# Kernel optimization log

Hardware: AMD Instinct MI355X
Metric: run time of the kernel (lower is better)

Reference implementation:

```python
import jax, jax.numpy as jnp
import numpy as np

B, S, H = 2, 2048, 2048
NH, NG = 16, 4           # attention heads, query groups
HD = H // NH             # head_dim = 128
HPG = NH // NG           # heads per group = 4


def setup_inputs() -> dict:
    key = jax.random.key(0)
    ks = jax.random.split(key, 8)
    s = 0.02
    return {
        "hidden_states": jax.random.normal(ks[0], (B, S, H), dtype=jnp.float32),
        "attention_mask": jnp.ones((B, S), dtype=jnp.int32),
        "Wq": jax.random.normal(ks[1], (H, H), dtype=jnp.float32) * s,
        "bq": jnp.zeros((H,), dtype=jnp.float32),
        "Wk": jax.random.normal(ks[2], (HD * NG, H), dtype=jnp.float32) * s,
        "bk": jnp.zeros((HD * NG,), dtype=jnp.float32),
        "Wv": jax.random.normal(ks[3], (HD * NG, H), dtype=jnp.float32) * s,
        "bv": jnp.zeros((HD * NG,), dtype=jnp.float32),
    }


def reference(hidden_states, attention_mask, Wq, bq, Wk, bk, Wv, bv):
    b, s, _ = hidden_states.shape
    scale = 1.0 / np.sqrt(HD).astype(np.float32)
    # projections (torch Linear: x @ W.T + b)
    q = hidden_states @ Wq.T + bq                      # [b,s,H]
    k = hidden_states @ Wk.T + bk                      # [b,s,NG*HD]
    v = hidden_states @ Wv.T + bv
    # q grouped so that repeat_interleave of k/v along heads == broadcast over heads_per_group
    q = q.reshape(b, s, NG, HPG, HD)                   # heads = group-major order
    k = k.reshape(b, s, NG, HD)
    v = v.reshape(b, s, NG, HD)
    scores = jnp.einsum("bsgpd,btgd->bgpst", q, k) * scale  # [b,NG,HPG,s,s]
    # mask: positions with attention_mask == 0 get finfo.min added
    mask_add = jnp.where(attention_mask == 0,
                         jnp.finfo(scores.dtype).min,
                         jnp.float32(0.0))             # [b,t]
    scores = scores + mask_add[:, None, None, None, :]
    attn = jax.nn.softmax(scores, axis=-1)             # dropout is identity in eval
    out = jnp.einsum("bgpst,btgd->bsgpd", attn, v)     # [b,s,NG,HPG,HD]
    return out.reshape(b, s, NH * HD)
```

## Files before the change

### kernel.cpp

```cpp
#include <hip/hip_runtime.h>
#include <hip/hip_bf16.h>

#define B_ 2
#define S_ 2048
#define H_ 2048
#define NH_ 16
#define NG_ 4
#define HD_ 128
#define HPG_ 4

typedef __attribute__((ext_vector_type(8))) short short8;
typedef __attribute__((ext_vector_type(4))) short short4v;
typedef __attribute__((ext_vector_type(4))) float float4v;

#define MFMA_BF16 __builtin_amdgcn_mfma_f32_16x16x32_bf16

#if __has_builtin(__builtin_amdgcn_exp2f)
#define EXP2(x) __builtin_amdgcn_exp2f(x)
#else
#define EXP2(x) exp2f(x)
#endif

__device__ __forceinline__ void gload16(const void* g, void* l) {
    __builtin_amdgcn_global_load_lds(
        (const __attribute__((address_space(1))) unsigned int*)g,
        (__attribute__((address_space(3))) unsigned int*)l, 16, 0, 0);
}

__device__ __forceinline__ short bf16bits(float f) {
    union { __hip_bfloat16 h; short s; } u;
    u.h = __float2bfloat16(f);
    return u.s;
}

__global__ __launch_bounds__(256) void cvt_all(const float* __restrict__ hs,
                                               const float* __restrict__ wq,
                                               const float* __restrict__ wk,
                                               const float* __restrict__ wv,
                                               const int* __restrict__ mask,
                                               const float* __restrict__ bq,
                                               const float* __restrict__ bk,
                                               const float* __restrict__ bv,
                                               __hip_bfloat16* __restrict__ o_hs,
                                               __hip_bfloat16* __restrict__ o_wq,
                                               __hip_bfloat16* __restrict__ o_wk,
                                               __hip_bfloat16* __restrict__ o_wv,
                                               float* __restrict__ o_m,
                                               float* __restrict__ o_bc) {
    int i = blockIdx.x * 256 + threadIdx.x;
    if (blockIdx.x == 0) {
#pragma unroll
        for (int j = 0; j < 16; ++j) {
            int idx = threadIdx.x * 16 + j;
            o_m[idx] = mask[idx] ? 0.0f : -3.0e38f;
        }
    }
    if (blockIdx.x == 1) {
#pragma unroll
        for (int j = 0; j < 12; ++j) {
            int idx = j * 256 + threadIdx.x;
            float v = (idx < 2048) ? bq[idx] : (idx < 2560) ? bk[idx - 2048] : bv[idx - 2560];
            o_bc[idx] = v;
        }
    }
    const float* src;
    __hip_bfloat16* dst;
    int off;
    if (i < 1048576)      { src = hs; dst = o_hs; off = i; }
    else if (i < 1572864) { src = wq; dst = o_wq; off = i - 1048576; }
    else if (i < 1703936) { src = wk; dst = o_wk; off = i - 1572864; }
    else                  { src = wv; dst = o_wv; off = i - 1703936; }
    const float4* s4 = (const float4*)src;
    float4 a = s4[2 * (size_t)off];
    float4 b = s4[2 * (size_t)off + 1];
    union { short8 s; __hip_bfloat16 h[8]; } u;
    u.h[0] = __float2bfloat16(a.x); u.h[1] = __float2bfloat16(a.y);
    u.h[2] = __float2bfloat16(a.z); u.h[3] = __float2bfloat16(a.w);
    u.h[4] = __float2bfloat16(b.x); u.h[5] = __float2bfloat16(b.y);
    u.h[6] = __float2bfloat16(b.z); u.h[7] = __float2bfloat16(b.w);
    *(short8*)(dst + 8 * (size_t)off) = u.s;
}

__global__ __launch_bounds__(512, 2) void gemm_qkv3(const __hip_bfloat16* __restrict__ A,
                                                    const __hip_bfloat16* __restrict__ Wcat,
                                                    const float* __restrict__ biasC,
                                                    __hip_bfloat16* __restrict__ qO,
                                                    __hip_bfloat16* __restrict__ kO,
                                                    __hip_bfloat16* __restrict__ vTO) {
    extern __shared__ char lds[];

    const int tid = threadIdx.x;
    const int lane = tid & 63;
    const int x = lane & 15, g = lane >> 4;
    const int wid = tid >> 6;
    const int wm = wid >> 2, wn = wid & 3;

    const int id0 = blockIdx.x;
    const int id = ((id0 & 7) << 5) | (id0 >> 3);
    const int bn_t = id >> 4, bm_t = id & 15;
    const int bm = bm_t * 256, bn = bn_t * 192;
    const int K = 2048;

    const int srow = tid >> 2;
    const int schunk = (tid & 3) ^ ((tid >> 3) & 3);
    const __hip_bfloat16* gA0 = A + (size_t)(bm + srow) * K + schunk * 8;
    const __hip_bfloat16* gA1 = A + (size_t)(bm + 128 + srow) * K + schunk * 8;
    const __hip_bfloat16* gB0 = Wcat + (size_t)(bn + srow) * K + schunk * 8;
    const __hip_bfloat16* gB1 = Wcat + (size_t)(bn + 128 + srow) * K + schunk * 8;
    const bool doB1 = (tid < 256);

    const int xk = (x >> 1) & 3;
    int aoffA[8], boffB[3];
#pragma unroll
    for (int mb = 0; mb < 8; ++mb)
        aoffA[mb] = (wm * 128 + mb * 16 + x) * 64 + ((g ^ xk) * 16);
#pragma unroll
    for (int nb = 0; nb < 3; ++nb)
        boffB[nb] = 16384 + (wn * 48 + nb * 16 + x) * 64 + ((g ^ xk) * 16);

    float4v acc[8][3];
#pragma unroll
    for (int i = 0; i < 8; ++i)
#pragma unroll
        for (int j = 0; j < 3; ++j) acc[i][j] = (float4v)0.f;

#pragma unroll
    for (int p = 0; p < 2; ++p) {
        char* stg = lds + p * 28672;
        gload16(gA0, stg + tid * 16);
        gload16(gA1, stg + 8192 + tid * 16);
        gload16(gB0, stg + 16384 + tid * 16);
        if (doB1) gload16(gB1, stg + 24576 + tid * 16);
        gA0 += 32; gA1 += 32; gB0 += 32; gB1 += 32;
    }
    if (doB1) asm volatile("s_waitcnt vmcnt(4)" ::: "memory");
    else      asm volatile("s_waitcnt vmcnt(3)" ::: "memory");
    __builtin_amdgcn_s_barrier();

#pragma unroll 4
    for (int t = 0; t < 64; ++t) {
        const char* bc = lds + (t & 3) * 28672;
        char* stg = lds + ((t + 2) & 3) * 28672;

        short8 afA[4], bfr[3];
#pragma unroll
        for (int mb = 0; mb < 4; ++mb) afA[mb] = *(const short8*)(bc + aoffA[mb]);
#pragma unroll
        for (int nb = 0; nb < 3; ++nb) bfr[nb] = *(const short8*)(bc + boffB[nb]);
        if (t < 62) {
            gload16(gA0, stg + tid * 16);
            gload16(gA1, stg + 8192 + tid * 16);
            gA0 += 32; gA1 += 32;
        }
        __builtin_amdgcn_s_barrier();
        asm volatile("s_waitcnt lgkmcnt(0)");
        __builtin_amdgcn_sched_barrier(0);
        __builtin_amdgcn_s_setprio(1);
#pragma unroll
        for (int mb = 0; mb < 4; ++mb)
#pragma unroll
            for (int nb = 0; nb < 3; ++nb)
                acc[mb][nb] = MFMA_BF16(afA[mb], bfr[nb], acc[mb][nb], 0, 0, 0);
        __builtin_amdgcn_s_setprio(0);
        __builtin_amdgcn_s_barrier();

        short8 afB[4];
#pragma unroll
        for (int mb = 0; mb < 4; ++mb) afB[mb] = *(const short8*)(bc + aoffA[4 + mb]);
        if (t < 62) {
            gload16(gB0, stg + 16384 + tid * 16);
            if (doB1) gload16(gB1, stg + 24576 + tid * 16);
            gB0 += 32; gB1 += 32;
        }
        __builtin_amdgcn_s_barrier();
        asm volatile("s_waitcnt lgkmcnt(0)");
        __builtin_amdgcn_sched_barrier(0);
        __builtin_amdgcn_s_setprio(1);
#pragma unroll
        for (int mb = 0; mb < 4; ++mb)
#pragma unroll
            for (int nb = 0; nb < 3; ++nb)
                acc[4 + mb][nb] = MFMA_BF16(afB[mb], bfr[nb], acc[4 + mb][nb], 0, 0, 0);
        __builtin_amdgcn_s_setprio(0);
        if (t < 62) {
            if (doB1) asm volatile("s_waitcnt vmcnt(4)" ::: "memory");
            else      asm volatile("s_waitcnt vmcnt(3)" ::: "memory");
        } else {
            asm volatile("s_waitcnt vmcnt(0)" ::: "memory");
        }
        __builtin_amdgcn_s_barrier();
    }

#pragma unroll
    for (int mb = 0; mb < 8; ++mb) {
#pragma unroll
        for (int nb = 0; nb < 3; ++nb) {
            const int n = bn + wn * 48 + nb * 16 + x;
            const float bsv = biasC[n];
            const int m0 = bm + wm * 128 + mb * 16 + g * 4;
            if (n < 2048) {
#pragma unroll
                for (int r = 0; r < 4; ++r)
                    qO[(size_t)(m0 + r) * 2048 + n] = __float2bfloat16(acc[mb][nb][r] + bsv);
            } else if (n < 2560) {
                const int nk = n - 2048;
#pragma unroll
                for (int r = 0; r < 4; ++r)
                    kO[(size_t)(m0 + r) * 512 + nk] = __float2bfloat16(acc[mb][nb][r] + bsv);
            } else {
                const int nv = n - 2560;
                const int gv = nv >> 7, d = nv & 127;
                const int bb2 = m0 >> 11, s = m0 & 2047;
                short4v pk;
#pragma unroll
                for (int r = 0; r < 4; ++r) pk[r] = bf16bits(acc[mb][nb][r] + bsv);
                *(short4v*)(vTO + ((size_t)(bb2 * NG_ + gv) * HD_ + d) * S_ + s) = pk;
            }
        }
    }
}

__global__ __launch_bounds__(512, 2) void attn(const __hip_bfloat16* __restrict__ q,
                                               const __hip_bfloat16* __restrict__ k,
                                               const __hip_bfloat16* __restrict__ vT,
                                               const float* __restrict__ M,
                                               float* __restrict__ out) {
    extern __shared__ char smem[];
    char* Ks = smem;
    char* Vs = smem + 16384;
    char* Ps = smem + 32768;

    const int tid = threadIdx.x;
    const int lane = tid & 63;
    const int w = tid >> 6;
    const int wm = w >> 2, wn = w & 3;
    const int x = lane & 15, g = lane >> 4;

    const int bid0 = blockIdx.x;
    const int bid = ((bid0 & 7) << 5) | (bid0 >> 3);
    const int qt = bid & 7;
    const int hp = (bid >> 3) & 3;
    const int gi = (bid >> 5) & 3;
    const int b = bid >> 7;
    const int head = gi * HPG_ + hp;
    const int q0 = qt * 256;

    short8 qf[4][4];
#pragma unroll
    for (int nb = 0; nb < 4; ++nb) {
        const int qq = q0 + wn * 64 + nb * 16 + x;
        const __hip_bfloat16* qrow = q + ((size_t)(b * S_ + qq) * NH_ + head) * HD_ + g * 8;
#pragma unroll
        for (int ks = 0; ks < 4; ++ks)
            qf[nb][ks] = *(const short8*)(qrow + ks * 32);
    }

    const int kchunk = (tid & 15) ^ ((tid >> 4) & 15);
    const __hip_bfloat16* kp = k + ((size_t)(b * S_ + (tid >> 4)) * NG_ + gi) * HD_ + kchunk * 8;
    const int vchunk = (tid & 7) ^ ((tid >> 3) & 7);
    const __hip_bfloat16* vp = vT + ((size_t)(b * NG_ + gi) * HD_ + (tid >> 3)) * S_ + vchunk * 8;
    const float* mp = M + b * S_ + wm * 32 + g * 4;

    float4v O[4][4];
#pragma unroll
    for (int i = 0; i < 4; ++i)
#pragma unroll
        for (int j = 0; j < 4; ++j) O[i][j] = (float4v)0.f;
    float l_part[4] = {0.f, 0.f, 0.f, 0.f};

    const float SM = 0.08838834764831845f * 1.4426950408889634f;

    gload16(kp, Ks + tid * 16);
    gload16(kp + 16384, Ks + tid * 16 + 8192);
    kp += 32768;

    for (int it = 0; it < 32; ++it) {
        __syncthreads();
        float4 mv0 = *(const float4*)(mp);
        float4 mv1 = *(const float4*)(mp + 16);
        mp += 64;
        gload16(vp, Vs + tid * 16);
        gload16(vp + 131072, Vs + tid * 16 + 8192);
        vp += 64;

        float4v sc[2][4];
#pragma unroll
        for (int i = 0; i < 2; ++i)
#pragma unroll
            for (int j = 0; j < 4; ++j) sc[i][j] = (float4v)0.f;
        __builtin_amdgcn_s_setprio(1);
#pragma unroll
        for (int ks = 0; ks < 4; ++ks) {
            short8 af0 = *(const short8*)(Ks + (wm * 32 + x) * 256 + (((ks * 4 + g) ^ x) * 16));
            short8 af1 = *(const short8*)(Ks + (wm * 32 + 16 + x) * 256 + (((ks * 4 + g) ^ x) * 16));
#pragma unroll
            for (int nb = 0; nb < 4; ++nb) {
                sc[0][nb] = MFMA_BF16(af0, qf[nb][ks], sc[0][nb], 0, 0, 0);
                sc[1][nb] = MFMA_BF16(af1, qf[nb][ks], sc[1][nb], 0, 0, 0);
            }
        }
        __builtin_amdgcn_s_setprio(0);

#pragma unroll
        for (int mb = 0; mb < 2; ++mb) {
            const float4 mv = mb ? mv1 : mv0;
            const int hs = wm * 8 + mb * 4 + g;
#pragma unroll
            for (int nb = 0; nb < 4; ++nb) {
                float p0 = EXP2(fmaf(sc[mb][nb][0], SM, mv.x));
                float p1 = EXP2(fmaf(sc[mb][nb][1], SM, mv.y));
                float p2 = EXP2(fmaf(sc[mb][nb][2], SM, mv.z));
                float p3 = EXP2(fmaf(sc[mb][nb][3], SM, mv.w));
                l_part[nb] += (p0 + p1) + (p2 + p3);
                short4v pk;
                pk[0] = bf16bits(p0); pk[1] = bf16bits(p1);
                pk[2] = bf16bits(p2); pk[3] = bf16bits(p3);
                *(short4v*)(Ps + (wn * 64 + nb * 16 + x) * 136 + hs * 8) = pk;
            }
        }

        __syncthreads();
        if (it < 31) {
            gload16(kp, Ks + tid * 16);
            gload16(kp + 16384, Ks + tid * 16 + 8192);
            kp += 32768;
        }

#pragma unroll
        for (int ks = 0; ks < 2; ++ks) {
            short8 vf[4], pf[4];
#pragma unroll
            for (int i4 = 0; i4 < 4; ++i4) {
                vf[i4] = *(const short8*)(Vs + (wm * 64 + i4 * 16 + x) * 128 +
                                          (((ks * 4 + g) ^ (x & 7)) * 16));
                const char* pb = Ps + (wn * 64 + i4 * 16 + x) * 136 + (8 * ks + 2 * g) * 8;
                union { short4v h[2]; short8 s8; } uu;
                uu.h[0] = *(const short4v*)pb;
                uu.h[1] = *(const short4v*)(pb + 8);
                pf[i4] = uu.s8;
            }
            __builtin_amdgcn_s_setprio(1);
#pragma unroll
            for (int mb = 0; mb < 4; ++mb)
#pragma unroll
                for (int nb = 0; nb < 4; ++nb)
                    O[mb][nb] = MFMA_BF16(vf[mb], pf[nb], O[mb][nb], 0, 0, 0);
            __builtin_amdgcn_s_setprio(0);
        }
    }

    __syncthreads();
#pragma unroll
    for (int nb = 0; nb < 4; ++nb) {
        l_part[nb] += __shfl_xor(l_part[nb], 16);
        l_part[nb] += __shfl_xor(l_part[nb], 32);
    }
    float* lws = (float*)Ps;
    if (g == 0) {
#pragma unroll
        for (int nb = 0; nb < 4; ++nb)
            lws[wm * 256 + wn * 64 + nb * 16 + x] = l_part[nb];
    }
    __syncthreads();
    float inv[4];
#pragma unroll
    for (int nb = 0; nb < 4; ++nb)
        inv[nb] = 1.0f / (l_part[nb] + lws[(wm ^ 1) * 256 + wn * 64 + nb * 16 + x]);

#pragma unroll
    for (int mb = 0; mb < 4; ++mb) {
#pragma unroll
        for (int nb = 0; nb < 4; ++nb) {
            const int qq = q0 + wn * 64 + nb * 16 + x;
            const int d0 = wm * 64 + mb * 16 + g * 4;
            float4v o = O[mb][nb] * inv[nb];
            *(float4v*)(out + (size_t)(b * S_ + qq) * H_ + head * HD_ + d0) = o;
        }
    }
}

extern "C" void kernel_launch(void* const* d_in, const int* in_sizes, int n_in,
                              void* d_out, int out_size, void* d_ws, size_t ws_size,
                              hipStream_t stream) {
    (void)in_sizes; (void)n_in; (void)out_size; (void)ws_size;
    const float* hs = (const float*)d_in[0];
    const int* amask = (const int*)d_in[1];
    const float* Wq = (const float*)d_in[2];
    const float* bq = (const float*)d_in[3];
    const float* Wk = (const float*)d_in[4];
    const float* bk = (const float*)d_in[5];
    const float* Wv = (const float*)d_in[6];
    const float* bv = (const float*)d_in[7];
    float* out = (float*)d_out;

    char* ws = (char*)d_ws;
    __hip_bfloat16* hsB = (__hip_bfloat16*)(ws);
    __hip_bfloat16* WqB = (__hip_bfloat16*)(ws + 16777216);
    __hip_bfloat16* WkB = (__hip_bfloat16*)(ws + 25165824);
    __hip_bfloat16* WvB = (__hip_bfloat16*)(ws + 27262976);
    __hip_bfloat16* qB  = (__hip_bfloat16*)(ws + 29360128);
    __hip_bfloat16* kB  = (__hip_bfloat16*)(ws + 46137344);
    __hip_bfloat16* vTB = (__hip_bfloat16*)(ws + 50331648);
    float* Mf           = (float*)(ws + 54525952);
    float* biasC        = (float*)(ws + 54542336);

    hipFuncSetAttribute((const void*)gemm_qkv3,
                        hipFuncAttributeMaxDynamicSharedMemorySize, 114688);
    hipFuncSetAttribute((const void*)attn,
                        hipFuncAttributeMaxDynamicSharedMemorySize, 67584);

    cvt_all<<<7168, 256, 0, stream>>>(hs, Wq, Wk, Wv, amask, bq, bk, bv,
                                      hsB, WqB, WkB, WvB, Mf, biasC);
    gemm_qkv3<<<256, 512, 114688, stream>>>(hsB, WqB, biasC, qB, kB, vTB);
    attn<<<256, 512, 67584, stream>>>(qB, kB, vTB, Mf, out);
}
```

Baseline: 232.7 us.

## Software-pipeline attention loop with double-buffered K, V and P tiles

Restructures the attention main loop so the QK^T and softmax for tile i run alongside the PV product for tile i-1. K, V and P get double buffers in LDS, which removes the second __syncthreads per iteration and lets loads for the next tile overlap compute. A prologue and epilogue handle the first and last tiles. LDS use roughly doubles to about 132 KB, so only one block fits per CU. With a 256-block grid this may not cost occupancy in practice.

```diff
diff --git a/kernel.cpp b/kernel.cpp
--- a/kernel.cpp
+++ b/kernel.cpp
@@ -227,8 +227,8 @@
                                                float* __restrict__ out) {
     extern __shared__ char smem[];
     char* Ks = smem;
-    char* Vs = smem + 16384;
-    char* Ps = smem + 32768;
+    char* Vs = smem + 32768;
+    char* Ps = smem + 65536;
 
     const int tid = threadIdx.x;
     const int lane = tid & 63;
@@ -267,23 +267,11 @@
 #pragma unroll
         for (int j = 0; j < 4; ++j) O[i][j] = (float4v)0.f;
     float l_part[4] = {0.f, 0.f, 0.f, 0.f};
+    float4v sc[2][4];
 
     const float SM = 0.08838834764831845f * 1.4426950408889634f;
 
-    gload16(kp, Ks + tid * 16);
-    gload16(kp + 16384, Ks + tid * 16 + 8192);
-    kp += 32768;
-
-    for (int it = 0; it < 32; ++it) {
-        __syncthreads();
-        float4 mv0 = *(const float4*)(mp);
-        float4 mv1 = *(const float4*)(mp + 16);
-        mp += 64;
-        gload16(vp, Vs + tid * 16);
-        gload16(vp + 131072, Vs + tid * 16 + 8192);
-        vp += 64;
-
-        float4v sc[2][4];
+    auto QKf = [&](const char* KsC) {
 #pragma unroll
         for (int i = 0; i < 2; ++i)
 #pragma unroll
@@ -291,8 +279,8 @@
         __builtin_amdgcn_s_setprio(1);
 #pragma unroll
         for (int ks = 0; ks < 4; ++ks) {
-            short8 af0 = *(const short8*)(Ks + (wm * 32 + x) * 256 + (((ks * 4 + g) ^ x) * 16));
-            short8 af1 = *(const short8*)(Ks + (wm * 32 + 16 + x) * 256 + (((ks * 4 + g) ^ x) * 16));
+            short8 af0 = *(const short8*)(KsC + (wm * 32 + x) * 256 + (((ks * 4 + g) ^ x) * 16));
+            short8 af1 = *(const short8*)(KsC + (wm * 32 + 16 + x) * 256 + (((ks * 4 + g) ^ x) * 16));
 #pragma unroll
             for (int nb = 0; nb < 4; ++nb) {
                 sc[0][nb] = MFMA_BF16(af0, qf[nb][ks], sc[0][nb], 0, 0, 0);
@@ -300,7 +288,33 @@
             }
         }
         __builtin_amdgcn_s_setprio(0);
-
+    };
+
+    auto PVf = [&](const char* VsP, const char* PsP) {
+#pragma unroll
+        for (int ks = 0; ks < 2; ++ks) {
+            short8 vf[4], pf[4];
+#pragma unroll
+            for (int i4 = 0; i4 < 4; ++i4) {
+                vf[i4] = *(const short8*)(VsP + (wm * 64 + i4 * 16 + x) * 128 +
+                                          (((ks * 4 + g) ^ (x & 7)) * 16));
+                const char* pb = PsP + (wn * 64 + i4 * 16 + x) * 136 + (8 * ks + 2 * g) * 8;
+                union { short4v h[2]; short8 s8; } uu;
+                uu.h[0] = *(const short4v*)pb;
+                uu.h[1] = *(const short4v*)(pb + 8);
+                pf[i4] = uu.s8;
+            }
+            __builtin_amdgcn_s_setprio(1);
+#pragma unroll
+            for (int mb = 0; mb < 4; ++mb)
+#pragma unroll
+                for (int nb = 0; nb < 4; ++nb)
+                    O[mb][nb] = MFMA_BF16(vf[mb], pf[nb], O[mb][nb], 0, 0, 0);
+            __builtin_amdgcn_s_setprio(0);
+        }
+    };
+
+    auto SMf = [&](char* PsC, float4 mv0, float4 mv1) {
 #pragma unroll
         for (int mb = 0; mb < 2; ++mb) {
             const float4 mv = mb ? mv1 : mv0;
@@ -315,41 +329,62 @@
                 short4v pk;
                 pk[0] = bf16bits(p0); pk[1] = bf16bits(p1);
                 pk[2] = bf16bits(p2); pk[3] = bf16bits(p3);
-                *(short4v*)(Ps + (wn * 64 + nb * 16 + x) * 136 + hs * 8) = pk;
+                *(short4v*)(PsC + (wn * 64 + nb * 16 + x) * 136 + hs * 8) = pk;
             }
         }
-
+    };
+
+    gload16(kp, Ks + tid * 16);
+    gload16(kp + 16384, Ks + tid * 16 + 8192);
+    kp += 32768;
+    __syncthreads();
+
+    {
+        float4 mv0 = *(const float4*)(mp);
+        float4 mv1 = *(const float4*)(mp + 16);
+        mp += 64;
+        gload16(vp, Vs + tid * 16);
+        gload16(vp + 131072, Vs + tid * 16 + 8192);
+        vp += 64;
+        QKf(Ks);
+        SMf(Ps, mv0, mv1);
+        gload16(kp, Ks + 16384 + tid * 16);
+        gload16(kp + 16384, Ks + 16384 + tid * 16 + 8192);
+        kp += 32768;
+    }
+
+#pragma unroll 2
+    for (int it = 1; it < 32; ++it) {
         __syncthreads();
+        const int p = it & 1;
+        char* KsC = Ks + p * 16384;
+        char* VsN = Vs + p * 16384;
+        char* VsP = Vs + (p ^ 1) * 16384;
+        char* PsC = Ps + p * 34816;
+        char* PsP = Ps + (p ^ 1) * 34816;
+
+        float4 mv0 = *(const float4*)(mp);
+        float4 mv1 = *(const float4*)(mp + 16);
+        mp += 64;
+        gload16(vp, VsN + tid * 16);
+        gload16(vp + 131072, VsN + tid * 16 + 8192);
+        vp += 64;
+
+        QKf(KsC);
+        PVf(VsP, PsP);
+        SMf(PsC, mv0, mv1);
+
         if (it < 31) {
-            gload16(kp, Ks + tid * 16);
-            gload16(kp + 16384, Ks + tid * 16 + 8192);
+            char* KsN = Ks + (p ^ 1) * 16384;
+            gload16(kp, KsN + tid * 16);
+            gload16(kp + 16384, KsN + tid * 16 + 8192);
             kp += 32768;
         }
-
-#pragma unroll
-        for (int ks = 0; ks < 2; ++ks) {
-            short8 vf[4], pf[4];
-#pragma unroll
-            for (int i4 = 0; i4 < 4; ++i4) {
-                vf[i4] = *(const short8*)(Vs + (wm * 64 + i4 * 16 + x) * 128 +
-                                          (((ks * 4 + g) ^ (x & 7)) * 16));
-                const char* pb = Ps + (wn * 64 + i4 * 16 + x) * 136 + (8 * ks + 2 * g) * 8;
-                union { short4v h[2]; short8 s8; } uu;
-                uu.h[0] = *(const short4v*)pb;
-                uu.h[1] = *(const short4v*)(pb + 8);
-                pf[i4] = uu.s8;
-            }
-            __builtin_amdgcn_s_setprio(1);
-#pragma unroll
-            for (int mb = 0; mb < 4; ++mb)
-#pragma unroll
-                for (int nb = 0; nb < 4; ++nb)
-                    O[mb][nb] = MFMA_BF16(vf[mb], pf[nb], O[mb][nb], 0, 0, 0);
-            __builtin_amdgcn_s_setprio(0);
-        }
     }
 
     __syncthreads();
+    PVf(Vs + 16384, Ps + 34816);
+
 #pragma unroll
     for (int nb = 0; nb < 4; ++nb) {
         l_part[nb] += __shfl_xor(l_part[nb], 16);
@@ -407,10 +442,10 @@
     hipFuncSetAttribute((const void*)gemm_qkv3,
                         hipFuncAttributeMaxDynamicSharedMemorySize, 114688);
     hipFuncSetAttribute((const void*)attn,
-                        hipFuncAttributeMaxDynamicSharedMemorySize, 67584);
+                        hipFuncAttributeMaxDynamicSharedMemorySize, 135168);
 
     cvt_all<<<7168, 256, 0, stream>>>(hs, Wq, Wk, Wv, amask, bq, bk, bv,
                                       hsB, WqB, WkB, WvB, Mf, biasC);
     gemm_qkv3<<<256, 512, 114688, stream>>>(hsB, WqB, biasC, qB, kB, vTB);
-    attn<<<256, 512, 67584, stream>>>(qB, kB, vTB, Mf, out);
-}
+    attn<<<256, 512, 135168, stream>>>(qB, kB, vTB, Mf, out);
+}
```

Measured after the change: 244.0 us. +4.9%, slower.
